# Optimization experiments

Measured on AMD Instinct MI355X. Metric: run time of the kernel, lower is better.

The kernel has to match this reference:

```python
import jax, jax.numpy as jnp
import numpy as np

C = 1024
R = 4            # reduction
A = 10           # num_adapters
LN_EPS = 1e-5
THRESHOLDS = np.array([1/9, 1/7, 1/5, 1/3, 1.0, 3.0, 5.0, 7.0, 9.0], dtype=np.float32)


def setup_inputs() -> dict:
    key = jax.random.key(0)
    k_feat, k_ar, k_w1, k_w2 = jax.random.split(key, 4)
    B, NA, H, W = 2, 3, 64, 64
    Cr = C // R
    output_feat = jax.random.normal(k_feat, (B, C, H, W), jnp.float32)
    # aspect ratios in [0,10) so all 10 adapters get selected
    aspect_ratio = jax.random.uniform(k_ar, (B, NA, H, W), jnp.float32) * 10.0
    # LayerNorm params (torch default init: weight=1, bias=0), stacked over adapters
    ln_scale = jnp.ones((A, C), jnp.float32)
    ln_bias = jnp.zeros((A, C), jnp.float32)
    # kaiming_normal_ fan_out / relu: std = sqrt(2/fan_out); torch weight [out,in]
    # w1 here is [C, Cr] == torch weight [Cr, C].T, fan_out = Cr
    w1 = jax.random.normal(k_w1, (A, C, Cr), jnp.float32) * np.sqrt(2.0 / Cr)
    # w2 here is [Cr, C] == torch weight [C, Cr].T, fan_out = C
    w2 = jax.random.normal(k_w2, (A, Cr, C), jnp.float32) * np.sqrt(2.0 / C)
    return dict(output_feat=output_feat, aspect_ratio=aspect_ratio,
                ln_scale=ln_scale, ln_bias=ln_bias, w1=w1, w2=w2)


def reference(output_feat, aspect_ratio, ln_scale, ln_bias, w1, w2):
    B, Cc, H, W = output_feat.shape
    NA = aspect_ratio.shape[1]
    HW = H * W
    # tokens [N, C]
    x = output_feat.transpose(0, 2, 3, 1).reshape(-1, Cc)
    # shared LayerNorm normalization (per-adapter affine applied after)
    mu = jnp.mean(x, axis=-1, keepdims=True)
    var = jnp.var(x, axis=-1, keepdims=True)
    norm = (x - mu) * jax.lax.rsqrt(var + LN_EPS)              # [N, C]
    y = norm[None, :, :] * ln_scale[:, None, :] + ln_bias[:, None, :]  # [A, N, C]
    h = jax.nn.gelu(jnp.einsum('anc,acd->and', y, w1), approximate=False)
    adapter_out = jnp.einsum('and,adc->anc', h, w2)            # [A, N, C]
    adapter_out = adapter_out.reshape(A, B, HW, Cc)            # [A, B, HW, C]
    # per-anchor, per-pixel adapter index from aspect ratio vs thresholds
    thr = jnp.asarray(THRESHOLDS, dtype=aspect_ratio.dtype)
    ar = aspect_ratio.reshape(B, NA, HW)
    idx = jnp.sum(ar[..., None] > thr, axis=-1)                # [B, NA, HW] in [0, 9]
    # gather selected adapter output per (batch, anchor, pixel)
    b_idx = jnp.arange(B)[:, None, None]
    p_idx = jnp.arange(HW)[None, None, :]
    selected = adapter_out[idx, b_idx, p_idx]                  # [B, NA, HW, C]
    selected = selected.mean(axis=1).reshape(B, H, W, Cc).transpose(0, 3, 1, 2)
    return selected + output_feat
```

## Files before the change

kernel.cpp:

```cpp
#include <hip/hip_runtime.h>
#include <hip/hip_bf16.h>
#include <math.h>

#define C_DIM 1024
#define CR    256
#define A_N   10
#define NANCH 3
#define B_N   2
#define HW_N  4096
#define NTOK  (B_N*HW_N)
#define KG2   (A_N*CR)

typedef unsigned short ushort_t;
typedef __attribute__((ext_vector_type(4))) float f32x4;
typedef __attribute__((ext_vector_type(8))) short bf16x8;

__device__ __forceinline__ ushort_t f2bf(float x) {
    __hip_bfloat16 h = __float2bfloat16(x);
    return *reinterpret_cast<ushort_t*>(&h);
}
__device__ __forceinline__ float bf2f(ushort_t u) {
    return __uint_as_float(((unsigned)u) << 16);
}

__device__ __forceinline__ float fast_gelu(float x) {
    float t = x * x;
    float u = x * (-1.5957691216f - 0.0713548163f * t);
    float e = __expf(u);
    return x * __frcp_rn(1.0f + e);
}

__global__ __launch_bounds__(256) void prep_all(
    const float* __restrict__ w1, const float* __restrict__ w2,
    const float* __restrict__ ln_s, const float* __restrict__ ln_b,
    const float* __restrict__ feat, const float* __restrict__ ar,
    ushort_t* __restrict__ w1t, ushort_t* __restrict__ w2t,
    float* __restrict__ bias1, float* __restrict__ sumv, float* __restrict__ sumq,
    int* __restrict__ cnt, int* __restrict__ tokw, int* __restrict__ tokmap) {
    __shared__ float lds[64][65];
    __shared__ float bb[4][64];
    __shared__ int lcnt[A_N], lpos[A_N], gbase[A_N];
    int id = blockIdx.x, tid = threadIdx.x;
    int lo = tid & 63, hi = tid >> 6;

    if (id < 640) {
        int d0 = (id & 3) * 64, c0 = ((id >> 2) & 15) * 64, a = id >> 6;
        #pragma unroll
        for (int i = 0; i < 16; i++) {
            int c_l = i * 4 + hi;
            lds[c_l][lo] = w1[((size_t)a * C_DIM + c0 + c_l) * CR + d0 + lo];
        }
        __syncthreads();
        {
            float s = 0.f;
            #pragma unroll
            for (int cc = 0; cc < 16; cc++) {
                int c = hi * 16 + cc;
                s += lds[c][lo] * ln_b[a * C_DIM + c0 + c];
            }
            bb[hi][lo] = s;
        }
        float sc = ln_s[a * C_DIM + c0 + lo];
        #pragma unroll
        for (int i = 0; i < 16; i++) {
            int d_l = i * 4 + hi;
            w1t[((size_t)a * CR + d0 + d_l) * C_DIM + c0 + lo] = f2bf(lds[lo][d_l] * sc);
        }
        __syncthreads();
        if (hi == 0)
            atomicAdd(&bias1[a * CR + d0 + lo], bb[0][lo] + bb[1][lo] + bb[2][lo] + bb[3][lo]);
    } else if (id < 1280) {
        int id2 = id - 640;
        int k0 = (id2 % 40) * 64, c0 = (id2 / 40) * 64;
        #pragma unroll
        for (int i = 0; i < 16; i++) {
            int k_l = i * 4 + hi;
            lds[k_l][lo] = w2[((size_t)k0 + k_l) * C_DIM + c0 + lo];
        }
        __syncthreads();
        #pragma unroll
        for (int i = 0; i < 16; i++) {
            int c_l = i * 4 + hi;
            w2t[((size_t)c0 + c_l) * KG2 + k0 + lo] = f2bf(lds[lo][c_l]);
        }
    } else if (id < 2304) {
        int id2 = id - 1280;
        int p0 = (id2 & 63) * 64, c0 = ((id2 >> 6) & 7) * 128, b = id2 >> 9;
        int p = lo, cs = hi;
        float s = 0.f, s2 = 0.f;
        #pragma unroll
        for (int c = cs; c < 128; c += 4) {
            float v = feat[((size_t)b * C_DIM + c0 + c) * HW_N + p0 + p];
            s += v; s2 += v * v;
        }
        float (*sh)[64] = (float(*)[64])lds;
        sh[cs][p] = s; sh[cs + 4][p] = s2;
        __syncthreads();
        if (tid < 64) {
            float ss = sh[0][tid] + sh[1][tid] + sh[2][tid] + sh[3][tid];
            float qq = sh[4][tid] + sh[5][tid] + sh[6][tid] + sh[7][tid];
            int t = b * HW_N + p0 + tid;
            atomicAdd(&sumv[t], ss);
            atomicAdd(&sumq[t], qq);
        }
    } else {
        if (tid < A_N) { lcnt[tid] = 0; lpos[tid] = 0; }
        __syncthreads();
        int t = (id - 2304) * 256 + tid;
        int b = t >> 12, p = t & (HW_N - 1);
        const float THR[9] = {1.0f/9.0f, 1.0f/7.0f, 0.2f, 1.0f/3.0f, 1.0f, 3.0f, 5.0f, 7.0f, 9.0f};
        int idxs[NANCH];
        #pragma unroll
        for (int na = 0; na < NANCH; na++) {
            float v = ar[(size_t)b * NANCH * HW_N + na * HW_N + p];
            int idx = 0;
            #pragma unroll
            for (int i = 0; i < 9; i++) idx += (v > THR[i]) ? 1 : 0;
            idxs[na] = idx;
        }
        int myA[NANCH], myC[NANCH], nmine = 0;
        #pragma unroll
        for (int j = 0; j < NANCH; j++) {
            bool first = true; int c3 = 0;
            #pragma unroll
            for (int k = 0; k < NANCH; k++) {
                if (idxs[k] == idxs[j]) { c3++; if (k < j) first = false; }
            }
            if (first) {
                myA[nmine] = idxs[j];
                myC[nmine] = c3;
                nmine++;
                atomicAdd(&lcnt[idxs[j]], 1);
            }
        }
        __syncthreads();
        if (tid < A_N) gbase[tid] = atomicAdd(&cnt[tid], lcnt[tid]);
        __syncthreads();
        for (int i = 0; i < NANCH; i++) {
            if (i < nmine) {
                int a2 = myA[i];
                int slot = atomicAdd(&lpos[a2], 1);
                int pos = gbase[a2] + slot;
                tokw[a2 * NTOK + pos] = t;
                tokmap[t * 3 + i] = pos | (a2 << 13) | (myC[i] << 17);
            } else {
                tokmap[t * 3 + i] = 0;
            }
        }
    }
}

__global__ __launch_bounds__(256) void normk(const float* __restrict__ feat,
                                             const float* __restrict__ sumv,
                                             const float* __restrict__ sumq,
                                             ushort_t* __restrict__ normG) {
    int p0 = blockIdx.x * 64, c0 = blockIdx.y * 64, b = blockIdx.z;
    __shared__ float lds[64][65];
    int tid = threadIdx.x, lo = tid & 63, hi = tid >> 6;
    #pragma unroll
    for (int i = 0; i < 16; i++) {
        int c_l = i * 4 + hi;
        lds[c_l][lo] = feat[((size_t)b * C_DIM + c0 + c_l) * HW_N + p0 + lo];
    }
    __syncthreads();
    int t_l = tid >> 3, cg = tid & 7;
    #pragma unroll
    for (int ii = 0; ii < 2; ii++) {
        int tl = ii * 32 + t_l;
        int t = b * HW_N + p0 + tl;
        float m = sumv[t] * (1.f / C_DIM);
        float q = sumq[t] * (1.f / C_DIM);
        float r = rsqrtf(q - m * m + 1e-5f);
        bf16x8 v;
        #pragma unroll
        for (int k = 0; k < 8; k++)
            v[k] = (short)f2bf((lds[cg * 8 + k][tl] - m) * r);
        *(bf16x8*)(normG + (size_t)t * C_DIM + c0 + cg * 8) = v;
    }
}

__device__ __forceinline__ void gemm_core_ptrs(
    const ushort_t* const ap[4], const ushort_t* const bp[4],
    int K, ushort_t* As, ushort_t* Bs, f32x4 acc[4][4]) {
    const int tid = threadIdx.x;
    const int lane = tid & 63;
    const int w = tid >> 6;
    const int wr = w >> 1, wc = w & 1;
    const int lrow = lane & 15;
    const int quad = lane >> 4;
    const int swzr = lrow & 7;

    #pragma unroll
    for (int i = 0; i < 4; i++)
        #pragma unroll
        for (int j = 0; j < 4; j++)
            #pragma unroll
            for (int e = 0; e < 4; e++) acc[i][j][e] = 0.f;

    for (int k0 = 0; k0 < K; k0 += 64) {
        __syncthreads();
        #pragma unroll
        for (int i = 0; i < 4; i++) {
            __builtin_amdgcn_global_load_lds(
                (__attribute__((address_space(1))) void*)(ap[i] + k0),
                (__attribute__((address_space(3))) void*)(As + (w * 32 + i * 8) * 64),
                16, 0, 0);
            __builtin_amdgcn_global_load_lds(
                (__attribute__((address_space(1))) void*)(bp[i] + k0),
                (__attribute__((address_space(3))) void*)(Bs + (w * 32 + i * 8) * 64),
                16, 0, 0);
        }
        __syncthreads();
        #pragma unroll
        for (int ks = 0; ks < 2; ks++) {
            const int cidx = ((ks * 4 + quad) ^ swzr) * 8;
            bf16x8 af[4], bfr[4];
            #pragma unroll
            for (int mt = 0; mt < 4; mt++)
                af[mt] = *(const bf16x8*)(As + (wr * 64 + mt * 16 + lrow) * 64 + cidx);
            #pragma unroll
            for (int nt = 0; nt < 4; nt++)
                bfr[nt] = *(const bf16x8*)(Bs + (wc * 64 + nt * 16 + lrow) * 64 + cidx);
            #pragma unroll
            for (int mt = 0; mt < 4; mt++)
                #pragma unroll
                for (int nt = 0; nt < 4; nt++)
                    acc[mt][nt] = __builtin_amdgcn_mfma_f32_16x16x32_bf16(af[mt], bfr[nt], acc[mt][nt], 0, 0, 0);
        }
    }
}

__device__ __forceinline__ void gemm_core_64(
    const ushort_t* const ap[2], const ushort_t* const bp[4],
    int K, ushort_t* As, ushort_t* Bs, f32x4 acc[4][2]) {
    const int tid = threadIdx.x;
    const int lane = tid & 63;
    const int w = tid >> 6;
    const int lrow = lane & 15;
    const int quad = lane >> 4;
    const int swzr = lrow & 7;

    #pragma unroll
    for (int i = 0; i < 4; i++)
        #pragma unroll
        for (int j = 0; j < 2; j++)
            #pragma unroll
            for (int e = 0; e < 4; e++) acc[i][j][e] = 0.f;

    for (int k0 = 0; k0 < K; k0 += 64) {
        __syncthreads();
        #pragma unroll
        for (int i = 0; i < 2; i++)
            __builtin_amdgcn_global_load_lds(
                (__attribute__((address_space(1))) void*)(ap[i] + k0),
                (__attribute__((address_space(3))) void*)(As + (w * 16 + i * 8) * 64),
                16, 0, 0);
        #pragma unroll
        for (int i = 0; i < 4; i++)
            __builtin_amdgcn_global_load_lds(
                (__attribute__((address_space(1))) void*)(bp[i] + k0),
                (__attribute__((address_space(3))) void*)(Bs + (w * 32 + i * 8) * 64),
                16, 0, 0);
        __syncthreads();
        #pragma unroll
        for (int ks = 0; ks < 2; ks++) {
            const int cidx = ((ks * 4 + quad) ^ swzr) * 8;
            bf16x8 af[4], bfr[2];
            #pragma unroll
            for (int mt = 0; mt < 4; mt++)
                af[mt] = *(const bf16x8*)(As + (mt * 16 + lrow) * 64 + cidx);
            #pragma unroll
            for (int nt = 0; nt < 2; nt++)
                bfr[nt] = *(const bf16x8*)(Bs + (w * 32 + nt * 16 + lrow) * 64 + cidx);
            #pragma unroll
            for (int mt = 0; mt < 4; mt++)
                #pragma unroll
                for (int nt = 0; nt < 2; nt++)
                    acc[mt][nt] = __builtin_amdgcn_mfma_f32_16x16x32_bf16(af[mt], bfr[nt], acc[mt][nt], 0, 0, 0);
        }
    }
}

__global__ __launch_bounds__(256) void gemm1c(const ushort_t* __restrict__ normG,
                                              const ushort_t* __restrict__ w1t,
                                              const float* __restrict__ bias1,
                                              const int* __restrict__ tokw,
                                              const int* __restrict__ cnt,
                                              ushort_t* __restrict__ Hc) {
    int a = blockIdx.z;
    int mcount = cnt[a];
    int m0 = blockIdx.y * 64;
    if (m0 >= mcount) return;
    int n0 = blockIdx.x * 128;
    int base = 0;
    for (int a2 = 0; a2 < a; a2++) base += cnt[a2];

    __shared__ __align__(16) ushort_t As[64 * 64];
    __shared__ __align__(16) ushort_t Bs[128 * 64];

    int tid = threadIdx.x, lane = tid & 63, w = tid >> 6;
    int lrow8 = lane >> 3;
    int scol = ((lane & 7) ^ lrow8) * 8;

    const ushort_t* ap[2];
    const ushort_t* bp[4];
    #pragma unroll
    for (int i = 0; i < 2; i++) {
        int rt = tokw[a * NTOK + m0 + w * 16 + i * 8 + lrow8] & (NTOK - 1);
        ap[i] = normG + (size_t)rt * C_DIM + scol;
    }
    #pragma unroll
    for (int i = 0; i < 4; i++)
        bp[i] = w1t + ((size_t)a * CR + n0 + w * 32 + i * 8 + lrow8) * C_DIM + scol;

    f32x4 acc[4][2];
    gemm_core_64(ap, bp, C_DIM, As, Bs, acc);

    int lrow = lane & 15, quad = lane >> 4;
    float bi[2];
    #pragma unroll
    for (int nt = 0; nt < 2; nt++)
        bi[nt] = bias1[a * CR + n0 + w * 32 + nt * 16 + lrow];
    #pragma unroll
    for (int mt = 0; mt < 4; mt++)
        #pragma unroll
        for (int r = 0; r < 4; r++) {
            int i_row = m0 + mt * 16 + quad * 4 + r;
            bool live = i_row < mcount;
            #pragma unroll
            for (int nt = 0; nt < 2; nt++) {
                int col = n0 + w * 32 + nt * 16 + lrow;
                float v = acc[mt][nt][r] + bi[nt];
                if (live)
                    Hc[(size_t)(base + i_row) * CR + col] = f2bf(fast_gelu(v));
            }
        }
}

__global__ __launch_bounds__(256) void gemm2c(const ushort_t* __restrict__ Hc,
                                              const ushort_t* __restrict__ w2t,
                                              const int* __restrict__ cnt,
                                              ushort_t* __restrict__ O) {
    int a = blockIdx.z;
    int mcount = cnt[a];
    int m0 = blockIdx.y * 128;
    if (m0 >= mcount) return;
    int n0 = blockIdx.x * 128;
    int base = 0;
    for (int a2 = 0; a2 < a; a2++) base += cnt[a2];

    __shared__ __align__(16) ushort_t As[128 * 64];
    __shared__ __align__(16) ushort_t Bs[128 * 64];

    int tid = threadIdx.x, lane = tid & 63, w = tid >> 6;
    int lrow8 = lane >> 3;
    int scol = ((lane & 7) ^ lrow8) * 8;
    int srowl = w * 32 + lrow8;

    const ushort_t* ap[4];
    const ushort_t* bp[4];
    #pragma unroll
    for (int i = 0; i < 4; i++) {
        ap[i] = Hc + (size_t)(base + m0 + srowl + i * 8) * CR + scol;
        bp[i] = w2t + (size_t)(n0 + srowl + i * 8) * KG2 + a * CR + scol;
    }

    f32x4 acc[4][4];
    gemm_core_ptrs(ap, bp, CR, As, Bs, acc);

    int wr = w >> 1, wc = w & 1, lrow = lane & 15, quad = lane >> 4;
    #pragma unroll
    for (int mt = 0; mt < 4; mt++)
        #pragma unroll
        for (int r = 0; r < 4; r++) {
            int i_row = m0 + wr * 64 + mt * 16 + quad * 4 + r;
            bool live = i_row < mcount;
            #pragma unroll
            for (int nt = 0; nt < 4; nt++) {
                int col = n0 + wc * 64 + nt * 16 + lrow;
                if (live)
                    O[(size_t)(base + i_row) * C_DIM + col] = f2bf(acc[mt][nt][r]);
            }
        }
}

__global__ __launch_bounds__(256) void finalk2(const ushort_t* __restrict__ O,
                                               const int* __restrict__ tokmap,
                                               const int* __restrict__ cnt,
                                               const float* __restrict__ feat,
                                               float* __restrict__ out) {
    int p0 = blockIdx.x * 64, c0 = blockIdx.y * 256, b = blockIdx.z;
    __shared__ float lds[64][260];
    __shared__ int pbase[A_N];
    int tid = threadIdx.x;
    if (tid < A_N) {
        int s = 0;
        for (int k = 0; k < tid; k++) s += cnt[k];
        pbase[tid] = s;
    }
    __syncthreads();
    int tl8 = tid >> 5, l32 = tid & 31;
    #pragma unroll
    for (int ii = 0; ii < 8; ii++) {
        int tl = ii * 8 + tl8;
        int t = b * HW_N + p0 + tl;
        float val8[8];
        #pragma unroll
        for (int k = 0; k < 8; k++) val8[k] = 0.f;
        #pragma unroll
        for (int j = 0; j < 3; j++) {
            int e = tokmap[t * 3 + j];
            float wv = (float)(e >> 17) * (1.0f / 3.0f);
            int a2 = (e >> 13) & 15;
            int row = pbase[a2] + (e & 8191);
            bf16x8 v = *(const bf16x8*)(O + (size_t)row * C_DIM + c0 + l32 * 8);
            #pragma unroll
            for (int k = 0; k < 8; k++)
                val8[k] += wv * bf2f((ushort_t)v[k]);
        }
        f32x4 v0 = {val8[0], val8[1], val8[2], val8[3]};
        f32x4 v1 = {val8[4], val8[5], val8[6], val8[7]};
        *(f32x4*)&lds[tl][l32 * 8] = v0;
        *(f32x4*)&lds[tl][l32 * 8 + 4] = v1;
    }
    __syncthreads();
    int lo = tid & 63, hi = tid >> 6;
    for (int i = 0; i < 64; i++) {
        int c_l = i * 4 + hi;
        size_t o = ((size_t)b * C_DIM + c0 + c_l) * HW_N + p0 + lo;
        out[o] = lds[lo][c_l] + feat[o];
    }
}

extern "C" void kernel_launch(void* const* d_in, const int* in_sizes, int n_in,
                              void* d_out, int out_size, void* d_ws, size_t ws_size,
                              hipStream_t stream) {
    (void)in_sizes; (void)n_in; (void)out_size; (void)ws_size;
    const float* feat = (const float*)d_in[0];
    const float* ar   = (const float*)d_in[1];
    const float* ln_s = (const float*)d_in[2];
    const float* ln_b = (const float*)d_in[3];
    const float* w1   = (const float*)d_in[4];
    const float* w2   = (const float*)d_in[5];
    float* out = (float*)d_out;
    char* ws = (char*)d_ws;

    float*    bias1  = (float*)(ws + 0);
    int*      cnt    = (int*)(ws + 10240);
    float*    sumv   = (float*)(ws + 10496);
    float*    sumq   = (float*)(ws + 43264);
    const size_t ZERO_BYTES = 76800;
    int*      tokmap = (int*)(ws + 76800);
    int*      tokw   = (int*)(ws + 175104);
    ushort_t* w1t    = (ushort_t*)(ws + 502784);
    ushort_t* w2t    = (ushort_t*)(ws + 5745664);
    ushort_t* normG  = (ushort_t*)(ws + 10988544);
    ushort_t* Hc     = (ushort_t*)(ws + 27765760);
    ushort_t* O      = (ushort_t*)(ws + 40414208);

    dim3 blk(256);
    hipMemsetAsync(ws, 0, ZERO_BYTES, stream);
    prep_all<<<dim3(2336), blk, 0, stream>>>(w1, w2, ln_s, ln_b, feat, ar,
                                             w1t, w2t, bias1, sumv, sumq, cnt, tokw, tokmap);
    normk<<<dim3(64, 16, B_N), blk, 0, stream>>>(feat, sumv, sumq, normG);
    gemm1c<<<dim3(2, 128, A_N), blk, 0, stream>>>(normG, w1t, bias1, tokw, cnt, Hc);
    gemm2c<<<dim3(8, 64, A_N), blk, 0, stream>>>(Hc, w2t, cnt, O);
    finalk2<<<dim3(64, 4, B_N), blk, 0, stream>>>(O, tokmap, cnt, feat, out);
}
```

Measured before the change: 100.5 us.

## Retile gemm1 to 128x64 with 2x2 waves and shrink final gather tiles

The first GEMM now uses 128-row by 64-column tiles with a 2x2 wave layout instead of 64x128 with four waves split along N. The intent is to cut per-block reloads of the gathered token rows and the W1 rows. Separately, the final gather/transpose kernel now covers 64 channels per block instead of 256, using a smaller padded LDS tile. That gives four times as many blocks for better occupancy and lower LDS use, at the cost of more blocks each re-reading the token map.

```diff
diff --git a/kernel.cpp b/kernel.cpp
--- a/kernel.cpp
+++ b/kernel.cpp
@@ -230,12 +230,13 @@
     }
 }
 
-__device__ __forceinline__ void gemm_core_64(
-    const ushort_t* const ap[2], const ushort_t* const bp[4],
+__device__ __forceinline__ void gemm_core_n64(
+    const ushort_t* const ap[4], const ushort_t* const bp[2],
     int K, ushort_t* As, ushort_t* Bs, f32x4 acc[4][2]) {
     const int tid = threadIdx.x;
     const int lane = tid & 63;
     const int w = tid >> 6;
+    const int wr = w >> 1, wc = w & 1;
     const int lrow = lane & 15;
     const int quad = lane >> 4;
     const int swzr = lrow & 7;
@@ -250,16 +251,16 @@
     for (int k0 = 0; k0 < K; k0 += 64) {
         __syncthreads();
         #pragma unroll
+        for (int i = 0; i < 4; i++)
+            __builtin_amdgcn_global_load_lds(
+                (__attribute__((address_space(1))) void*)(ap[i] + k0),
+                (__attribute__((address_space(3))) void*)(As + (w * 32 + i * 8) * 64),
+                16, 0, 0);
+        #pragma unroll
         for (int i = 0; i < 2; i++)
             __builtin_amdgcn_global_load_lds(
-                (__attribute__((address_space(1))) void*)(ap[i] + k0),
-                (__attribute__((address_space(3))) void*)(As + (w * 16 + i * 8) * 64),
-                16, 0, 0);
-        #pragma unroll
-        for (int i = 0; i < 4; i++)
-            __builtin_amdgcn_global_load_lds(
                 (__attribute__((address_space(1))) void*)(bp[i] + k0),
-                (__attribute__((address_space(3))) void*)(Bs + (w * 32 + i * 8) * 64),
+                (__attribute__((address_space(3))) void*)(Bs + (w * 16 + i * 8) * 64),
                 16, 0, 0);
         __syncthreads();
         #pragma unroll
@@ -268,10 +269,10 @@
             bf16x8 af[4], bfr[2];
             #pragma unroll
             for (int mt = 0; mt < 4; mt++)
-                af[mt] = *(const bf16x8*)(As + (mt * 16 + lrow) * 64 + cidx);
+                af[mt] = *(const bf16x8*)(As + (wr * 64 + mt * 16 + lrow) * 64 + cidx);
             #pragma unroll
             for (int nt = 0; nt < 2; nt++)
-                bfr[nt] = *(const bf16x8*)(Bs + (w * 32 + nt * 16 + lrow) * 64 + cidx);
+                bfr[nt] = *(const bf16x8*)(Bs + (wc * 32 + nt * 16 + lrow) * 64 + cidx);
             #pragma unroll
             for (int mt = 0; mt < 4; mt++)
                 #pragma unroll
@@ -289,47 +290,47 @@
                                               ushort_t* __restrict__ Hc) {
     int a = blockIdx.z;
     int mcount = cnt[a];
-    int m0 = blockIdx.y * 64;
+    int m0 = blockIdx.y * 128;
     if (m0 >= mcount) return;
-    int n0 = blockIdx.x * 128;
+    int n0 = blockIdx.x * 64;
     int base = 0;
     for (int a2 = 0; a2 < a; a2++) base += cnt[a2];
 
-    __shared__ __align__(16) ushort_t As[64 * 64];
-    __shared__ __align__(16) ushort_t Bs[128 * 64];
+    __shared__ __align__(16) ushort_t As[128 * 64];
+    __shared__ __align__(16) ushort_t Bs[64 * 64];
 
     int tid = threadIdx.x, lane = tid & 63, w = tid >> 6;
     int lrow8 = lane >> 3;
     int scol = ((lane & 7) ^ lrow8) * 8;
 
-    const ushort_t* ap[2];
-    const ushort_t* bp[4];
-    #pragma unroll
-    for (int i = 0; i < 2; i++) {
-        int rt = tokw[a * NTOK + m0 + w * 16 + i * 8 + lrow8] & (NTOK - 1);
+    const ushort_t* ap[4];
+    const ushort_t* bp[2];
+    #pragma unroll
+    for (int i = 0; i < 4; i++) {
+        int rt = tokw[a * NTOK + m0 + w * 32 + i * 8 + lrow8] & (NTOK - 1);
         ap[i] = normG + (size_t)rt * C_DIM + scol;
     }
     #pragma unroll
-    for (int i = 0; i < 4; i++)
-        bp[i] = w1t + ((size_t)a * CR + n0 + w * 32 + i * 8 + lrow8) * C_DIM + scol;
+    for (int i = 0; i < 2; i++)
+        bp[i] = w1t + ((size_t)a * CR + n0 + w * 16 + i * 8 + lrow8) * C_DIM + scol;
 
     f32x4 acc[4][2];
-    gemm_core_64(ap, bp, C_DIM, As, Bs, acc);
-
-    int lrow = lane & 15, quad = lane >> 4;
+    gemm_core_n64(ap, bp, C_DIM, As, Bs, acc);
+
+    int wr = w >> 1, wc = w & 1, lrow = lane & 15, quad = lane >> 4;
     float bi[2];
     #pragma unroll
     for (int nt = 0; nt < 2; nt++)
-        bi[nt] = bias1[a * CR + n0 + w * 32 + nt * 16 + lrow];
+        bi[nt] = bias1[a * CR + n0 + wc * 32 + nt * 16 + lrow];
     #pragma unroll
     for (int mt = 0; mt < 4; mt++)
         #pragma unroll
         for (int r = 0; r < 4; r++) {
-            int i_row = m0 + mt * 16 + quad * 4 + r;
+            int i_row = m0 + wr * 64 + mt * 16 + quad * 4 + r;
             bool live = i_row < mcount;
             #pragma unroll
             for (int nt = 0; nt < 2; nt++) {
-                int col = n0 + w * 32 + nt * 16 + lrow;
+                int col = n0 + wc * 32 + nt * 16 + lrow;
                 float v = acc[mt][nt][r] + bi[nt];
                 if (live)
                     Hc[(size_t)(base + i_row) * CR + col] = f2bf(fast_gelu(v));
@@ -389,20 +390,20 @@
                                                const int* __restrict__ cnt,
                                                const float* __restrict__ feat,
                                                float* __restrict__ out) {
-    int p0 = blockIdx.x * 64, c0 = blockIdx.y * 256, b = blockIdx.z;
-    __shared__ float lds[64][260];
+    int p0 = blockIdx.x * 64, c0 = blockIdx.y * 64, b = blockIdx.z;
+    __shared__ float lds[64][65];
     __shared__ int pbase[A_N];
-    int tid = threadIdx.x;
+    int tid = threadIdx.x, lo = tid & 63, hi = tid >> 6;
     if (tid < A_N) {
         int s = 0;
         for (int k = 0; k < tid; k++) s += cnt[k];
         pbase[tid] = s;
     }
     __syncthreads();
-    int tl8 = tid >> 5, l32 = tid & 31;
-    #pragma unroll
-    for (int ii = 0; ii < 8; ii++) {
-        int tl = ii * 8 + tl8;
+    int t_l = tid >> 3, cg = tid & 7;
+    #pragma unroll
+    for (int ii = 0; ii < 2; ii++) {
+        int tl = ii * 32 + t_l;
         int t = b * HW_N + p0 + tl;
         float val8[8];
         #pragma unroll
@@ -413,19 +414,18 @@
             float wv = (float)(e >> 17) * (1.0f / 3.0f);
             int a2 = (e >> 13) & 15;
             int row = pbase[a2] + (e & 8191);
-            bf16x8 v = *(const bf16x8*)(O + (size_t)row * C_DIM + c0 + l32 * 8);
+            bf16x8 v = *(const bf16x8*)(O + (size_t)row * C_DIM + c0 + cg * 8);
             #pragma unroll
             for (int k = 0; k < 8; k++)
                 val8[k] += wv * bf2f((ushort_t)v[k]);
         }
-        f32x4 v0 = {val8[0], val8[1], val8[2], val8[3]};
-        f32x4 v1 = {val8[4], val8[5], val8[6], val8[7]};
-        *(f32x4*)&lds[tl][l32 * 8] = v0;
-        *(f32x4*)&lds[tl][l32 * 8 + 4] = v1;
+        #pragma unroll
+        for (int k = 0; k < 8; k++)
+            lds[tl][cg * 8 + k] = val8[k];
     }
     __syncthreads();
-    int lo = tid & 63, hi = tid >> 6;
-    for (int i = 0; i < 64; i++) {
+    #pragma unroll
+    for (int i = 0; i < 16; i++) {
         int c_l = i * 4 + hi;
         size_t o = ((size_t)b * C_DIM + c0 + c_l) * HW_N + p0 + lo;
         out[o] = lds[lo][c_l] + feat[o];
@@ -463,7 +463,7 @@
     prep_all<<<dim3(2336), blk, 0, stream>>>(w1, w2, ln_s, ln_b, feat, ar,
                                              w1t, w2t, bias1, sumv, sumq, cnt, tokw, tokmap);
     normk<<<dim3(64, 16, B_N), blk, 0, stream>>>(feat, sumv, sumq, normG);
-    gemm1c<<<dim3(2, 128, A_N), blk, 0, stream>>>(normG, w1t, bias1, tokw, cnt, Hc);
+    gemm1c<<<dim3(4, 64, A_N), blk, 0, stream>>>(normG, w1t, bias1, tokw, cnt, Hc);
     gemm2c<<<dim3(8, 64, A_N), blk, 0, stream>>>(Hc, w2t, cnt, O);
-    finalk2<<<dim3(64, 4, B_N), blk, 0, stream>>>(O, tokmap, cnt, feat, out);
-}
+    finalk2<<<dim3(64, 16, B_N), blk, 0, stream>>>(O, tokmap, cnt, feat, out);
+}
```

Result: slower. 104.4 us (+3.9%).
